# Kernel tuning notes

Measured on AMD Instinct MI355X. Metric: run time of the kernel, lower is better.

## Reference

```python
import jax, jax.numpy as jnp
import numpy as np

N = 100000   # nodes
E = 3200000  # edges (before self-loops)
G = 256      # graphs in batch
IN_DIM, HID, OUT3 = 25, 64, 32


def setup_inputs() -> dict:
    key = jax.random.key(0)
    ks = jax.random.split(key, 13)
    def w(k, shape, fan_in):
        return jax.random.normal(k, shape, jnp.float32) * (1.0 / np.sqrt(fan_in))
    return {
        "x": jax.random.normal(ks[0], (N, IN_DIM), jnp.float32),
        "edge_index": jax.random.randint(ks[1], (2, E), 0, N, dtype=jnp.int32),
        "batch": jnp.sort(jax.random.randint(ks[2], (N,), 0, G, dtype=jnp.int32)),
        "W1": w(ks[3], (IN_DIM, HID), IN_DIM), "b1": jnp.zeros((HID,), jnp.float32),
        "W2": w(ks[4], (HID, HID), HID),       "b2": jnp.zeros((HID,), jnp.float32),
        "W3": w(ks[5], (HID, OUT3), HID),      "b3": jnp.zeros((OUT3,), jnp.float32),
        "Wh1": w(ks[6], (OUT3, 32), OUT3),     "bh1": jnp.zeros((32,), jnp.float32),
        "Wh2": w(ks[7], (32, 1), 32),          "bh2": jnp.zeros((1,), jnp.float32),
    }


def _gcn_layer(x, W, b, src, dst, num_nodes):
    # GCNConv: h = W^T x; out_i = sum_j norm_ij * h_j (+ self-loop), norm = d_i^-1/2 d_j^-1/2
    h = x @ W  # [N, F_out]
    ones = jnp.ones(src.shape[0], h.dtype)
    deg = jax.ops.segment_sum(ones, dst, num_segments=num_nodes)  # includes self-loops -> >= 1
    dinv = jax.lax.rsqrt(jnp.maximum(deg, 1.0))
    norm = dinv[src] * dinv[dst]                       # [E+N]
    msgs = h[src] * norm[:, None]                       # gather + scale
    out = jax.ops.segment_sum(msgs, dst, num_segments=num_nodes)  # scatter-add
    return out + b


def reference(x, edge_index, batch, W1, b1, W2, b2, W3, b3, Wh1, bh1, Wh2, bh2):
    n = x.shape[0]
    loops = jnp.arange(n, dtype=edge_index.dtype)
    src = jnp.concatenate([edge_index[0], loops])  # add self-loops
    dst = jnp.concatenate([edge_index[1], loops])

    h = jax.nn.relu(_gcn_layer(x, W1, b1, src, dst, n))
    h = jax.nn.relu(_gcn_layer(h, W2, b2, src, dst, n))
    h = jax.nn.relu(_gcn_layer(h, W3, b3, src, dst, n))

    # global mean pool over graphs
    counts = jax.ops.segment_sum(jnp.ones(n, h.dtype), batch, num_segments=G)
    g = jax.ops.segment_sum(h, batch, num_segments=G) / jnp.maximum(counts, 1.0)[:, None]

    y = jax.nn.relu(g @ Wh1 + bh1) @ Wh2 + bh2  # [G, 1]
    return y.squeeze(-1)
```

## Files before the change

### kernel.cpp

```cpp
#include <hip/hip_runtime.h>
#include <hip/hip_fp16.h>


#define IN_DIM 25
#define HID 64
#define OUT3 32
#define BK_LOG 7
#define BK_NODES 128
#define MAXB 1024
#define EPB1 16384
#define BCAP 8192

__device__ inline int ld_nt_i32(const int* p) {
    return __builtin_nontemporal_load(p);
}

__global__ __launch_bounds__(256) void bucket_hist(const int* __restrict__ dst,
                                                   int* __restrict__ bhist, int nE) {
    __shared__ int h[MAXB];
    for (int i = threadIdx.x; i < MAXB; i += 256) h[i] = 0;
    __syncthreads();
    int e0 = blockIdx.x * 8192;
    int cnt = min(8192, nE - e0);
    for (int i = threadIdx.x; i < cnt; i += 256)
        atomicAdd(&h[(unsigned)dst[e0 + i] >> BK_LOG], 1);
    __syncthreads();
    for (int i = threadIdx.x; i < MAXB; i += 256)
        if (h[i]) atomicAdd(&bhist[i], h[i]);
}

__global__ __launch_bounds__(256) void bucket_scan(const int* __restrict__ bhist,
                                                   int* __restrict__ bbase,
                                                   int* __restrict__ cursor,
                                                   int* __restrict__ row_ptr,
                                                   int nb, int nE, int nN) {
    __shared__ int s4[256];
    int t = threadIdx.x;
    int v[4]; int sum = 0;
#pragma unroll
    for (int j = 0; j < 4; ++j) {
        int b = 4 * t + j;
        v[j] = (b < nb) ? bhist[b] : 0;
        sum += v[j];
    }
    s4[t] = sum;
    __syncthreads();
    for (int off = 1; off < 256; off <<= 1) {
        int mine = s4[t];
        int add = (t >= off) ? s4[t - off] : 0;
        __syncthreads();
        s4[t] = mine + add;
        __syncthreads();
    }
    int run = s4[t] - sum;
#pragma unroll
    for (int j = 0; j < 4; ++j) {
        int b = 4 * t + j;
        if (b < nb) { bbase[b] = run; cursor[b] = run; }
        run += v[j];
    }
    if (t == 0) { bbase[nb] = nE; row_ptr[nN] = nE; }
}

__global__ __launch_bounds__(256) void partition_kernel(
        const int* __restrict__ src, const int* __restrict__ dst,
        int* __restrict__ cursor, unsigned int* __restrict__ ebuf, int nE) {
    __shared__ int lh[MAXB];
    __shared__ int lrun[MAXB];
    __shared__ int lcur[MAXB];
    __shared__ int swp[256];
    __shared__ unsigned int stg[EPB1];
    __shared__ unsigned short sbk[EPB1];
    int t = threadIdx.x;
    int e0 = blockIdx.x * EPB1;
    int cnt = min(EPB1, nE - e0);
    for (int i = t; i < MAXB; i += 256) lh[i] = 0;
    __syncthreads();
    for (int i = t; i < cnt; i += 256)
        atomicAdd(&lh[(unsigned)dst[e0 + i] >> BK_LOG], 1);
    __syncthreads();
    int v[4]; int sum = 0;
#pragma unroll
    for (int j = 0; j < 4; ++j) { v[j] = lh[4 * t + j]; sum += v[j]; }
    swp[t] = sum;
    __syncthreads();
    for (int off = 1; off < 256; off <<= 1) {
        int mine = swp[t];
        int add = (t >= off) ? swp[t - off] : 0;
        __syncthreads();
        swp[t] = mine + add;
        __syncthreads();
    }
    int run = swp[t] - sum;
#pragma unroll
    for (int j = 0; j < 4; ++j) {
        int b = 4 * t + j;
        lh[b] = run;
        lcur[b] = 0;
        if (v[j] > 0) lrun[b] = atomicAdd(&cursor[b], v[j]);
        run += v[j];
    }
    __syncthreads();
    for (int i = t; i < cnt; i += 256) {
        int d = dst[e0 + i];
        int s = src[e0 + i];
        int b = (unsigned)d >> BK_LOG;
        int lp = atomicAdd(&lcur[b], 1);
        int slot = lh[b] + lp;
        stg[slot] = ((unsigned)(d & (BK_NODES - 1)) << 17) | (unsigned)s;
        sbk[slot] = (unsigned short)b;
    }
    __syncthreads();
    for (int i = t; i < cnt; i += 256) {
        int b = sbk[i];
        int g = lrun[b] + (i - lh[b]);
        ebuf[g] = stg[i];
    }
}

__global__ __launch_bounds__(256) void bucket_csr_kernel(
        unsigned int* __restrict__ ebuf, const int* __restrict__ bbase,
        float* __restrict__ dinv, int* __restrict__ row_ptr, int nN) {
    int b = blockIdx.x;
    int node_lo = b << BK_LOG;
    int nn = min(BK_NODES, nN - node_lo);
    int base = bbase[b];
    int cnt = bbase[b + 1] - base;
    if (cnt > BCAP) cnt = BCAP;
    __shared__ unsigned int in[BCAP];
    __shared__ unsigned int outb[BCAP];
    __shared__ int h[BK_NODES], sc[BK_NODES], lc[BK_NODES];
    int t = threadIdx.x;
    for (int i = t; i < cnt; i += 256) in[i] = ebuf[base + i];
    if (t < BK_NODES) { h[t] = 0; lc[t] = 0; }
    __syncthreads();
    for (int i = t; i < cnt; i += 256) atomicAdd(&h[in[i] >> 17], 1);
    __syncthreads();
    if (t < BK_NODES) sc[t] = h[t];
    __syncthreads();
    for (int off = 1; off < BK_NODES; off <<= 1) {
        int val = 0;
        if (t < BK_NODES) { val = sc[t]; if (t >= off) val += sc[t - off]; }
        __syncthreads();
        if (t < BK_NODES) sc[t] = val;
        __syncthreads();
    }
    if (t < BK_NODES && t < nn) {
        dinv[node_lo + t] = rsqrtf((float)h[t] + 1.0f);
        row_ptr[node_lo + t] = base + (sc[t] - h[t]);
    }
    __syncthreads();
    for (int i = t; i < cnt; i += 256) {
        unsigned int w = in[i];
        int dl = w >> 17;
        int lp = atomicAdd(&lc[dl], 1);
        outb[(sc[dl] - h[dl]) + lp] = w & 0x1FFFFu;
    }
    __syncthreads();
    for (int i = t; i < cnt; i += 256) ebuf[base + i] = outb[i];
}

__global__ void padx_kernel(const float* __restrict__ x, const float* __restrict__ dinv,
                            __half* __restrict__ xp, int n) {
    int i = blockIdx.x * 256 + threadIdx.x;
    if (i < n * 16) {
        int node = i >> 4, c2 = (i & 15) * 2;
        float s = dinv[node];
        float v0 = (c2     < IN_DIM) ? x[(size_t)node * IN_DIM + c2    ] * s : 0.f;
        float v1 = (c2 + 1 < IN_DIM) ? x[(size_t)node * IN_DIM + c2 + 1] * s : 0.f;
        *(__half2*)&xp[(size_t)node * 32 + c2] = __floats2half2_rn(v0, v1);
    }
}

__global__ void padw_kernel(const float* __restrict__ W1, float* __restrict__ W1p) {
    int i = blockIdx.x * 256 + threadIdx.x;
    if (i < 32 * HID) {
        int r = i >> 6, c = i & 63;
        W1p[i] = (r < IN_DIM) ? W1[r * HID + c] : 0.f;
    }
}

template<int INF, int OUTF, bool ACT, bool SCALE>
__global__ __launch_bounds__(256) void gemm_kernel(
        const float* __restrict__ in, const float* __restrict__ W,
        const float* __restrict__ bias, const float* __restrict__ dinv,
        void* __restrict__ out, int n) {
    constexpr int TPN = OUTF / 4;
    constexpr int NPB = 256 / TPN;
    constexpr int LDK = INF + 4;
    __shared__ float sW[INF * OUTF];
    __shared__ float sIn[NPB][LDK];
    for (int i = threadIdx.x; i < INF * OUTF; i += 256) sW[i] = W[i];
    int node0 = blockIdx.x * NPB;
    for (int i = threadIdx.x; i < NPB * INF; i += 256) {
        int ln = i / INF, k = i % INF;
        int node = node0 + ln;
        sIn[ln][k] = (node < n) ? in[(size_t)node * INF + k] : 0.f;
    }
    __syncthreads();
    int g   = threadIdx.x / TPN;
    int of0 = (threadIdx.x % TPN) * 4;
    int node = node0 + g;
    float4 acc = make_float4(0.f, 0.f, 0.f, 0.f);
#pragma unroll
    for (int k = 0; k < INF; ++k) {
        float aj = sIn[g][k];
        const float4 wv = *(const float4*)&sW[k * OUTF + of0];
        acc.x += aj * wv.x; acc.y += aj * wv.y;
        acc.z += aj * wv.z; acc.w += aj * wv.w;
    }
    if (ACT) {
        const float4 bv = *(const float4*)&bias[of0];
        acc.x = fmaxf(acc.x + bv.x, 0.f);
        acc.y = fmaxf(acc.y + bv.y, 0.f);
        acc.z = fmaxf(acc.z + bv.z, 0.f);
        acc.w = fmaxf(acc.w + bv.w, 0.f);
    }
    if (node < n) {
        if (SCALE) {
            float s = dinv[node];
            union { __half2 h[2]; uint2 u; } pk;
            pk.h[0] = __floats2half2_rn(acc.x * s, acc.y * s);
            pk.h[1] = __floats2half2_rn(acc.z * s, acc.w * s);
            *(uint2*)((__half*)out + (size_t)node * OUTF + of0) = pk.u;
        } else {
            *(float4*)((float*)out + (size_t)node * OUTF + of0) = acc;
        }
    }
}

template<int F, bool ACT>
__global__ __launch_bounds__(256) void gather_kernel(
        const __half* __restrict__ hp, const float* __restrict__ dinv,
        const int* __restrict__ row_ptr, const int* __restrict__ col,
        const float* __restrict__ bias, float* __restrict__ agg, int n) {
    constexpr int NPW = 64 / F;
    int wid  = (blockIdx.x * 256 + threadIdx.x) >> 6;
    int lane = threadIdx.x & 63;
    int sub  = lane / F;
    int f    = lane % F;
    int node = wid * NPW + sub;
    if (node >= n) return;
    float a0 = __half2float(hp[(size_t)node * F + f]);
    float a1 = 0.f, a2 = 0.f, a3 = 0.f;
    int e = row_ptr[node], end = row_ptr[node + 1];
    for (; e + 16 <= end; e += 16) {
        int c[16];
#pragma unroll
        for (int j = 0; j < 16; ++j) c[j] = ld_nt_i32(&col[e + j]);
        float v[16];
#pragma unroll
        for (int j = 0; j < 16; ++j) v[j] = __half2float(hp[(size_t)c[j] * F + f]);
#pragma unroll
        for (int j = 0; j < 4; ++j) {
            a0 += v[4 * j];     a1 += v[4 * j + 1];
            a2 += v[4 * j + 2]; a3 += v[4 * j + 3];
        }
    }
    for (; e + 4 <= end; e += 4) {
        int c0 = ld_nt_i32(&col[e]),     c1 = ld_nt_i32(&col[e + 1]);
        int c2 = ld_nt_i32(&col[e + 2]), c3 = ld_nt_i32(&col[e + 3]);
        a0 += __half2float(hp[(size_t)c0 * F + f]);
        a1 += __half2float(hp[(size_t)c1 * F + f]);
        a2 += __half2float(hp[(size_t)c2 * F + f]);
        a3 += __half2float(hp[(size_t)c3 * F + f]);
    }
    for (; e < end; ++e) a0 += __half2float(hp[(size_t)ld_nt_i32(&col[e]) * F + f]);
    float acc = ((a0 + a1) + (a2 + a3)) * dinv[node];
    float r = ACT ? fmaxf(acc + bias[f], 0.f) : acc;
    agg[(size_t)node * F + f] = r;
}

__global__ __launch_bounds__(256) void pool_kernel(
        const float* __restrict__ h3, const int* __restrict__ batch,
        int n, float* __restrict__ pool) {
    int g = blockIdx.x;
    int lo = 0, hi = n;
    while (lo < hi) { int m = (lo + hi) >> 1; if (batch[m] < g) lo = m + 1; else hi = m; }
    int s = lo;
    hi = n;
    while (lo < hi) { int m = (lo + hi) >> 1; if (batch[m] < g + 1) lo = m + 1; else hi = m; }
    int e = lo;
    constexpr int F = OUT3;
    int ln = threadIdx.x / F;
    int f  = threadIdx.x % F;
    float acc = 0.f;
    for (int i = s + ln; i < e; i += 8)
        acc += h3[(size_t)i * F + f];
    __shared__ float red[8][F];
    red[ln][f] = acc;
    __syncthreads();
    if (ln == 0) {
        float t = 0.f;
#pragma unroll
        for (int j = 0; j < 8; ++j) t += red[j][f];
        float cnt = (float)((e - s) > 0 ? (e - s) : 1);
        pool[g * F + f] = t / cnt;
    }
}

__global__ __launch_bounds__(256) void head_kernel(
        const float* __restrict__ pool, const float* __restrict__ Wh1,
        const float* __restrict__ bh1, const float* __restrict__ Wh2,
        const float* __restrict__ bh2, float* __restrict__ out) {
    __shared__ float sW1[32 * 32];
    __shared__ float sb1[32];
    __shared__ float sW2[32];
    int t = threadIdx.x;
    for (int i = t; i < 1024; i += 256) sW1[i] = Wh1[i];
    if (t < 32) { sb1[t] = bh1[t]; sW2[t] = Wh2[t]; }
    __syncthreads();
    int g = t;
    float y = bh2[0];
    const float* p = &pool[g * 32];
#pragma unroll 4
    for (int j = 0; j < 32; ++j) {
        float a = sb1[j];
#pragma unroll
        for (int k = 0; k < 32; ++k) a += p[k] * sW1[k * 32 + j];
        y += fmaxf(a, 0.f) * sW2[j];
    }
    out[g] = y;
}

extern "C" void kernel_launch(void* const* d_in, const int* in_sizes, int n_in,
                              void* d_out, int out_size, void* d_ws, size_t ws_size,
                              hipStream_t stream) {
    const float* x    = (const float*)d_in[0];
    const int*   ei   = (const int*)  d_in[1];
    const int*   batch= (const int*)  d_in[2];
    const float* W1   = (const float*)d_in[3];
    const float* b1   = (const float*)d_in[4];
    const float* W2   = (const float*)d_in[5];
    const float* b2   = (const float*)d_in[6];
    const float* W3   = (const float*)d_in[7];
    const float* b3   = (const float*)d_in[8];
    const float* Wh1  = (const float*)d_in[9];
    const float* bh1  = (const float*)d_in[10];
    const float* Wh2  = (const float*)d_in[11];
    const float* bh2  = (const float*)d_in[12];
    float* out = (float*)d_out;

    const int N = in_sizes[0] / IN_DIM;
    const int E = in_sizes[1] / 2;
    const int* src = ei;
    const int* dst = ei + E;
    const int NB = (N + BK_NODES - 1) >> BK_LOG;

    char* base = (char*)d_ws;
    unsigned int* ebuf = (unsigned int*)base;       base += (size_t)E * 4;
    int*   bhist   = (int*)base;                    base += (size_t)MAXB * 4;
    int*   bbase   = (int*)base;                    base += (size_t)(MAXB + 1) * 4;
    int*   cursor  = (int*)base;                    base += (size_t)MAXB * 4;
    int*   row_ptr = (int*)base;                    base += (size_t)(N + 1) * 4;
    float* dinv    = (float*)base;                  base += (size_t)N * 4;
    float* W1p     = (float*)base;                  base += (size_t)32 * HID * 4;
    float* bufA    = (float*)base;                  base += (size_t)N * HID * 4;
    float* bufB    = (float*)base;                  base += (size_t)N * HID * 4;
    float* pool    = (float*)base;

    hipMemsetAsync(bhist, 0, (size_t)MAXB * sizeof(int), stream);
    bucket_hist<<<(E + 8191) / 8192, 256, 0, stream>>>(dst, bhist, E);
    bucket_scan<<<1, 256, 0, stream>>>(bhist, bbase, cursor, row_ptr, NB, E, N);
    partition_kernel<<<(E + EPB1 - 1) / EPB1, 256, 0, stream>>>(src, dst, cursor, ebuf, E);
    bucket_csr_kernel<<<NB, 256, 0, stream>>>(ebuf, bbase, dinv, row_ptr, N);
    const int* col = (const int*)ebuf;

    padx_kernel<<<((size_t)N * 16 + 255) / 256, 256, 0, stream>>>(x, dinv, (__half*)bufB, N);
    padw_kernel<<<(32 * HID + 255) / 256, 256, 0, stream>>>(W1, W1p);
    gather_kernel<32, false><<<(N + 7) / 8, 256, 0, stream>>>((const __half*)bufB, dinv, row_ptr, col, nullptr, bufA, N);
    gemm_kernel<32, HID, true, false><<<(N + 15) / 16, 256, 0, stream>>>(bufA, W1p, b1, nullptr, bufB, N);

    gemm_kernel<HID, HID, false, true><<<(N + 15) / 16, 256, 0, stream>>>(bufB, W2, nullptr, dinv, bufA, N);
    gather_kernel<HID, true><<<(N + 3) / 4, 256, 0, stream>>>((const __half*)bufA, dinv, row_ptr, col, b2, bufB, N);

    gemm_kernel<HID, OUT3, false, true><<<(N + 31) / 32, 256, 0, stream>>>(bufB, W3, nullptr, dinv, bufA, N);
    gather_kernel<OUT3, true><<<(N + 7) / 8, 256, 0, stream>>>((const __half*)bufA, dinv, row_ptr, col, b3, bufB, N);

    pool_kernel<<<256, 256, 0, stream>>>(bufB, batch, N, pool);
    head_kernel<<<1, 256, 0, stream>>>(pool, Wh1, bh1, Wh2, bh2, out);
}
```

Before: 499.7 us.

## Split CSR rows into source ranges and gather in lockstep range sweeps

The CSR build now sub-sorts each node's edges into 8 source-index ranges and emits 9 row-pointer arrays (rps) in place of a single row_ptr. The gather kernel walks all of its nodes one source range at a time, with a block barrier between ranges, so concurrent waves hit a narrower slice of the feature table and should get better L2 locality. Each lane also handles a half2 feature pair and K nodes, and occupancy is raised via launch bounds. The cost is more row-pointer traffic and barriers, fewer lanes per node, and more serial work per thread.

```diff
diff --git a/kernel.cpp b/kernel.cpp
--- a/kernel.cpp
+++ b/kernel.cpp
@@ -10,6 +10,9 @@
 #define MAXB 1024
 #define EPB1 16384
 #define BCAP 8192
+#define RNG_LOG 14
+#define NR 8
+#define NKEY (BK_NODES * NR)
 
 __device__ inline int ld_nt_i32(const int* p) {
     return __builtin_nontemporal_load(p);
@@ -32,8 +35,7 @@
 __global__ __launch_bounds__(256) void bucket_scan(const int* __restrict__ bhist,
                                                    int* __restrict__ bbase,
                                                    int* __restrict__ cursor,
-                                                   int* __restrict__ row_ptr,
-                                                   int nb, int nE, int nN) {
+                                                   int nb, int nE) {
     __shared__ int s4[256];
     int t = threadIdx.x;
     int v[4]; int sum = 0;
@@ -59,7 +61,7 @@
         if (b < nb) { bbase[b] = run; cursor[b] = run; }
         run += v[j];
     }
-    if (t == 0) { bbase[nb] = nE; row_ptr[nN] = nE; }
+    if (t == 0) bbase[nb] = nE;
 }
 
 __global__ __launch_bounds__(256) void partition_kernel(
@@ -120,7 +122,7 @@
 
 __global__ __launch_bounds__(256) void bucket_csr_kernel(
         unsigned int* __restrict__ ebuf, const int* __restrict__ bbase,
-        float* __restrict__ dinv, int* __restrict__ row_ptr, int nN) {
+        float* __restrict__ dinv, int* __restrict__ rps, int nN) {
     int b = blockIdx.x;
     int node_lo = b << BK_LOG;
     int nn = min(BK_NODES, nN - node_lo);
@@ -129,32 +131,50 @@
     if (cnt > BCAP) cnt = BCAP;
     __shared__ unsigned int in[BCAP];
     __shared__ unsigned int outb[BCAP];
-    __shared__ int h[BK_NODES], sc[BK_NODES], lc[BK_NODES];
+    __shared__ int h[NKEY], sc[NKEY], lc[NKEY];
+    __shared__ int swp[256];
     int t = threadIdx.x;
     for (int i = t; i < cnt; i += 256) in[i] = ebuf[base + i];
-    if (t < BK_NODES) { h[t] = 0; lc[t] = 0; }
-    __syncthreads();
-    for (int i = t; i < cnt; i += 256) atomicAdd(&h[in[i] >> 17], 1);
-    __syncthreads();
-    if (t < BK_NODES) sc[t] = h[t];
-    __syncthreads();
-    for (int off = 1; off < BK_NODES; off <<= 1) {
-        int val = 0;
-        if (t < BK_NODES) { val = sc[t]; if (t >= off) val += sc[t - off]; }
-        __syncthreads();
-        if (t < BK_NODES) sc[t] = val;
-        __syncthreads();
-    }
-    if (t < BK_NODES && t < nn) {
-        dinv[node_lo + t] = rsqrtf((float)h[t] + 1.0f);
-        row_ptr[node_lo + t] = base + (sc[t] - h[t]);
-    }
+    for (int i = t; i < NKEY; i += 256) { h[i] = 0; lc[i] = 0; }
     __syncthreads();
     for (int i = t; i < cnt; i += 256) {
         unsigned int w = in[i];
-        int dl = w >> 17;
-        int lp = atomicAdd(&lc[dl], 1);
-        outb[(sc[dl] - h[dl]) + lp] = w & 0x1FFFFu;
+        int kk = (int)((w >> 17) << 3) | (int)((w & 0x1FFFFu) >> RNG_LOG);
+        atomicAdd(&h[kk], 1);
+    }
+    __syncthreads();
+    int v[4]; int sum = 0;
+#pragma unroll
+    for (int j = 0; j < 4; ++j) { v[j] = h[4 * t + j]; sum += v[j]; }
+    swp[t] = sum;
+    __syncthreads();
+    for (int off = 1; off < 256; off <<= 1) {
+        int mine = swp[t];
+        int add = (t >= off) ? swp[t - off] : 0;
+        __syncthreads();
+        swp[t] = mine + add;
+        __syncthreads();
+    }
+    int run = swp[t] - sum;
+#pragma unroll
+    for (int j = 0; j < 4; ++j) { sc[4 * t + j] = run; run += v[j]; }
+    __syncthreads();
+    for (int kk = t; kk < NKEY; kk += 256) {
+        int dl = kk >> 3;
+        if (dl < nn) rps[(size_t)(kk & 7) * nN + node_lo + dl] = base + sc[kk];
+    }
+    if (t < BK_NODES && t < nn) {
+        int s0 = sc[t << 3];
+        int e7 = sc[(t << 3) + 7] + h[(t << 3) + 7];
+        rps[(size_t)8 * nN + node_lo + t] = base + e7;
+        dinv[node_lo + t] = rsqrtf((float)(e7 - s0) + 1.0f);
+    }
+    __syncthreads();
+    for (int i = t; i < cnt; i += 256) {
+        unsigned int w = in[i];
+        int kk = (int)((w >> 17) << 3) | (int)((w & 0x1FFFFu) >> RNG_LOG);
+        int lp = atomicAdd(&lc[kk], 1);
+        outb[sc[kk] + lp] = w & 0x1FFFFu;
     }
     __syncthreads();
     for (int i = t; i < cnt; i += 256) ebuf[base + i] = outb[i];
@@ -229,46 +249,70 @@
     }
 }
 
-template<int F, bool ACT>
-__global__ __launch_bounds__(256) void gather_kernel(
+template<int F, bool ACT, int K>
+__global__ __launch_bounds__(256, 8) void gather_kernel(
         const __half* __restrict__ hp, const float* __restrict__ dinv,
-        const int* __restrict__ row_ptr, const int* __restrict__ col,
+        const int* __restrict__ rps, const int* __restrict__ col,
         const float* __restrict__ bias, float* __restrict__ agg, int n) {
-    constexpr int NPW = 64 / F;
+    constexpr int LPN = F / 2;
+    constexpr int SPW = 64 / LPN;
     int wid  = (blockIdx.x * 256 + threadIdx.x) >> 6;
     int lane = threadIdx.x & 63;
-    int sub  = lane / F;
-    int f    = lane % F;
-    int node = wid * NPW + sub;
-    if (node >= n) return;
-    float a0 = __half2float(hp[(size_t)node * F + f]);
-    float a1 = 0.f, a2 = 0.f, a3 = 0.f;
-    int e = row_ptr[node], end = row_ptr[node + 1];
-    for (; e + 16 <= end; e += 16) {
-        int c[16];
-#pragma unroll
-        for (int j = 0; j < 16; ++j) c[j] = ld_nt_i32(&col[e + j]);
-        float v[16];
-#pragma unroll
-        for (int j = 0; j < 16; ++j) v[j] = __half2float(hp[(size_t)c[j] * F + f]);
-#pragma unroll
-        for (int j = 0; j < 4; ++j) {
-            a0 += v[4 * j];     a1 += v[4 * j + 1];
-            a2 += v[4 * j + 2]; a3 += v[4 * j + 3];
+    int sub  = lane / LPN;
+    int f2   = lane % LPN;
+    int n0   = (wid * SPW + sub) * K;
+    float ax[K], ay[K];
+#pragma unroll
+    for (int k = 0; k < K; ++k) {
+        ax[k] = 0.f; ay[k] = 0.f;
+        int nk = n0 + k;
+        if (nk < n) {
+            float2 v = __half22float2(*(const __half2*)&hp[(size_t)nk * F + 2 * f2]);
+            ax[k] = v.x; ay[k] = v.y;
         }
     }
-    for (; e + 4 <= end; e += 4) {
-        int c0 = ld_nt_i32(&col[e]),     c1 = ld_nt_i32(&col[e + 1]);
-        int c2 = ld_nt_i32(&col[e + 2]), c3 = ld_nt_i32(&col[e + 3]);
-        a0 += __half2float(hp[(size_t)c0 * F + f]);
-        a1 += __half2float(hp[(size_t)c1 * F + f]);
-        a2 += __half2float(hp[(size_t)c2 * F + f]);
-        a3 += __half2float(hp[(size_t)c3 * F + f]);
-    }
-    for (; e < end; ++e) a0 += __half2float(hp[(size_t)ld_nt_i32(&col[e]) * F + f]);
-    float acc = ((a0 + a1) + (a2 + a3)) * dinv[node];
-    float r = ACT ? fmaxf(acc + bias[f], 0.f) : acc;
-    agg[(size_t)node * F + f] = r;
+    for (int r = 0; r < NR; ++r) {
+        const int* rs = rps + (size_t)r * n;
+        const int* re = rps + (size_t)(r + 1) * n;
+#pragma unroll
+        for (int k = 0; k < K; ++k) {
+            int nk = n0 + k;
+            if (nk < n) {
+                int e = rs[nk], e1 = re[nk];
+                for (; e + 4 <= e1; e += 4) {
+                    int c0 = ld_nt_i32(&col[e]);
+                    int c1 = ld_nt_i32(&col[e + 1]);
+                    int c2 = ld_nt_i32(&col[e + 2]);
+                    int c3 = ld_nt_i32(&col[e + 3]);
+                    float2 v0 = __half22float2(*(const __half2*)&hp[(size_t)c0 * F + 2 * f2]);
+                    float2 v1 = __half22float2(*(const __half2*)&hp[(size_t)c1 * F + 2 * f2]);
+                    float2 v2 = __half22float2(*(const __half2*)&hp[(size_t)c2 * F + 2 * f2]);
+                    float2 v3 = __half22float2(*(const __half2*)&hp[(size_t)c3 * F + 2 * f2]);
+                    ax[k] += (v0.x + v1.x) + (v2.x + v3.x);
+                    ay[k] += (v0.y + v1.y) + (v2.y + v3.y);
+                }
+                for (; e < e1; ++e) {
+                    int c = ld_nt_i32(&col[e]);
+                    float2 v = __half22float2(*(const __half2*)&hp[(size_t)c * F + 2 * f2]);
+                    ax[k] += v.x; ay[k] += v.y;
+                }
+            }
+        }
+        __syncthreads();
+    }
+#pragma unroll
+    for (int k = 0; k < K; ++k) {
+        int nk = n0 + k;
+        if (nk < n) {
+            float s = dinv[nk];
+            float rx = ax[k] * s, ry = ay[k] * s;
+            if (ACT) {
+                rx = fmaxf(rx + bias[2 * f2], 0.f);
+                ry = fmaxf(ry + bias[2 * f2 + 1], 0.f);
+            }
+            *(float2*)&agg[(size_t)nk * F + 2 * f2] = make_float2(rx, ry);
+        }
+    }
 }
 
 __global__ __launch_bounds__(256) void pool_kernel(
@@ -352,7 +396,7 @@
     int*   bhist   = (int*)base;                    base += (size_t)MAXB * 4;
     int*   bbase   = (int*)base;                    base += (size_t)(MAXB + 1) * 4;
     int*   cursor  = (int*)base;                    base += (size_t)MAXB * 4;
-    int*   row_ptr = (int*)base;                    base += (size_t)(N + 1) * 4;
+    int*   rps     = (int*)base;                    base += (size_t)(NR + 1) * N * 4;
     float* dinv    = (float*)base;                  base += (size_t)N * 4;
     float* W1p     = (float*)base;                  base += (size_t)32 * HID * 4;
     float* bufA    = (float*)base;                  base += (size_t)N * HID * 4;
@@ -361,21 +405,27 @@
 
     hipMemsetAsync(bhist, 0, (size_t)MAXB * sizeof(int), stream);
     bucket_hist<<<(E + 8191) / 8192, 256, 0, stream>>>(dst, bhist, E);
-    bucket_scan<<<1, 256, 0, stream>>>(bhist, bbase, cursor, row_ptr, NB, E, N);
+    bucket_scan<<<1, 256, 0, stream>>>(bhist, bbase, cursor, NB, E);
     partition_kernel<<<(E + EPB1 - 1) / EPB1, 256, 0, stream>>>(src, dst, cursor, ebuf, E);
-    bucket_csr_kernel<<<NB, 256, 0, stream>>>(ebuf, bbase, dinv, row_ptr, N);
+    bucket_csr_kernel<<<NB, 256, 0, stream>>>(ebuf, bbase, dinv, rps, N);
     const int* col = (const int*)ebuf;
+
+    constexpr int K64 = 7, K32 = 4;
+    const int npb64 = 4 * 2 * K64;
+    const int npb32 = 4 * 4 * K32;
+    const int blocks64 = (N + npb64 - 1) / npb64;
+    const int blocks32 = (N + npb32 - 1) / npb32;
 
     padx_kernel<<<((size_t)N * 16 + 255) / 256, 256, 0, stream>>>(x, dinv, (__half*)bufB, N);
     padw_kernel<<<(32 * HID + 255) / 256, 256, 0, stream>>>(W1, W1p);
-    gather_kernel<32, false><<<(N + 7) / 8, 256, 0, stream>>>((const __half*)bufB, dinv, row_ptr, col, nullptr, bufA, N);
+    gather_kernel<32, false, K32><<<blocks32, 256, 0, stream>>>((const __half*)bufB, dinv, rps, col, nullptr, bufA, N);
     gemm_kernel<32, HID, true, false><<<(N + 15) / 16, 256, 0, stream>>>(bufA, W1p, b1, nullptr, bufB, N);
 
     gemm_kernel<HID, HID, false, true><<<(N + 15) / 16, 256, 0, stream>>>(bufB, W2, nullptr, dinv, bufA, N);
-    gather_kernel<HID, true><<<(N + 3) / 4, 256, 0, stream>>>((const __half*)bufA, dinv, row_ptr, col, b2, bufB, N);
+    gather_kernel<HID, true, K64><<<blocks64, 256, 0, stream>>>((const __half*)bufA, dinv, rps, col, b2, bufB, N);
 
     gemm_kernel<HID, OUT3, false, true><<<(N + 31) / 32, 256, 0, stream>>>(bufB, W3, nullptr, dinv, bufA, N);
-    gather_kernel<OUT3, true><<<(N + 7) / 8, 256, 0, stream>>>((const __half*)bufA, dinv, row_ptr, col, b3, bufB, N);
+    gather_kernel<OUT3, true, K32><<<blocks32, 256, 0, stream>>>((const __half*)bufA, dinv, rps, col, b3, bufB, N);
 
     pool_kernel<<<256, 256, 0, stream>>>(bufB, batch, N, pool);
     head_kernel<<<1, 256, 0, stream>>>(pool, Wh1, bh1, Wh2, bh2, out);
```

Result: slower. 711.8 us (+42.4%).
